# Kernel optimization log

Measured on AMD Instinct MI355X. Metric: run time of the kernel, lower is better.

## Reference

```python
import jax, jax.numpy as jnp
from jax import lax
import numpy as np

B, N, S, K = 8, 4096, 1024, 32
D_FEAT = 64
EPS = 1e-5


def fps_idx(pts, npoint):
    # pts: [N,3] -> farthest point sampling indices [npoint] (deterministic start at 0)
    n = pts.shape[0]
    def body(i, state):
        dist, far, idxs = state
        idxs = idxs.at[i].set(far)
        d = jnp.sum((pts - pts[far]) ** 2, axis=-1)
        dist = jnp.minimum(dist, d)
        return dist, jnp.argmax(dist).astype(jnp.int32), idxs
    init = (jnp.full((n,), 1e10, pts.dtype), jnp.int32(0), jnp.zeros((npoint,), jnp.int32))
    _, _, idxs = lax.fori_loop(0, npoint, body, init)
    return idxs


def bn(x, g, b, axes, c_axis):
    # batch-norm, training mode (batch statistics), matching torch default module state
    m = jnp.mean(x, axes, keepdims=True)
    v = jnp.var(x, axes, keepdims=True)
    shape = [1] * x.ndim
    shape[c_axis] = -1
    return g.reshape(shape) * (x - m) * lax.rsqrt(v + EPS) + b.reshape(shape)


def conv1x1(x, w, b):
    # x: [B,C,S,K], w: [O,C], b: [O]
    return jnp.einsum('oc,bcsk->bosk', w, x) + b[None, :, None, None]


def setup_inputs():
    key = jax.random.key(0)
    ks = jax.random.split(key, 20)
    p = lambda k, shape: jax.random.normal(k, shape, jnp.float32) * 0.05
    inp = {
        'xyz': jax.random.normal(ks[0], (B, 3, N), jnp.float32),
        'features': jax.random.normal(ks[1], (B, D_FEAT, N), jnp.float32),
        # main MLP: 67 -> 64 -> 64 -> 128
        'w0': p(ks[2], (64, 67)), 'b0': p(ks[3], (64,)), 'g0': jnp.ones(64), 'be0': jnp.zeros(64),
        'w1': p(ks[4], (64, 64)), 'b1': p(ks[5], (64,)), 'g1': jnp.ones(64), 'be1': jnp.zeros(64),
        'w2': p(ks[6], (128, 64)), 'b2': p(ks[7], (128,)), 'g2': jnp.ones(128), 'be2': jnp.zeros(128),
        # WeightNet: 3 -> 8 -> 8 -> 16
        'ww0': p(ks[8], (8, 3)), 'wb0': p(ks[9], (8,)), 'wg0': jnp.ones(8), 'wbe0': jnp.zeros(8),
        'ww1': p(ks[10], (8, 8)), 'wb1': p(ks[11], (8,)), 'wg1': jnp.ones(8), 'wbe1': jnp.zeros(8),
        'ww2': p(ks[12], (16, 8)), 'wb2': p(ks[13], (16,)), 'wg2': jnp.ones(16), 'wbe2': jnp.zeros(16),
        # final linear 16*128 -> 128 and BN1d
        'lw': p(ks[14], (128, 16 * 128)), 'lb': p(ks[15], (128,)),
        'lg': jnp.ones(128), 'lbe': jnp.zeros(128),
    }
    return inp


def reference(xyz, features, w0, b0, g0, be0, w1, b1, g1, be1, w2, b2, g2, be2,
              ww0, wb0, wg0, wbe0, ww1, wb1, wg1, wbe1, ww2, wb2, wg2, wbe2,
              lw, lb, lg, lbe):
    xyz_t = jnp.transpose(xyz, (0, 2, 1))          # [B,N,3]
    feat_t = jnp.transpose(features, (0, 2, 1))    # [B,N,D]

    # farthest point sampling (indices non-differentiable, as in CUDA FPS)
    fidx = jax.vmap(lambda pts: fps_idx(pts, S))(lax.stop_gradient(xyz_t))  # [B,S]
    fps_xyz = jnp.take_along_axis(xyz_t, fidx[..., None], axis=1)           # [B,S,3]

    # KNN: squared distances [B,S,N], take K smallest
    d2 = (jnp.sum(fps_xyz ** 2, -1, keepdims=True)
          + jnp.sum(xyz_t ** 2, -1)[:, None, :]
          - 2.0 * jnp.einsum('bsc,bnc->bsn', fps_xyz, xyz_t))
    _, idx = lax.top_k(-lax.stop_gradient(d2), K)                            # [B,S,K]

    gather = jax.vmap(lambda src, i: src[i])
    grouped_xyz = gather(xyz_t, idx) - fps_xyz[:, :, None, :]                # [B,S,K,3]
    grouped_feat = gather(feat_t, idx)                                       # [B,S,K,D]
    nf = jnp.concatenate([grouped_xyz, grouped_feat], axis=-1)               # [B,S,K,3+D]

    nf = jnp.transpose(nf, (0, 3, 1, 2))                                     # [B,C,S,K]
    for w, b, g, be in ((w0, b0, g0, be0), (w1, b1, g1, be1), (w2, b2, g2, be2)):
        nf = jax.nn.relu(bn(conv1x1(nf, w, b), g, be, (0, 2, 3), 1))

    gx = jnp.transpose(grouped_xyz, (0, 3, 1, 2))                            # [B,3,S,K]
    wts = gx
    for w, b, g, be in ((ww0, wb0, wg0, wbe0), (ww1, wb1, wg1, wbe1), (ww2, wb2, wg2, wbe2)):
        wts = jax.nn.relu(bn(conv1x1(wts, w, b), g, be, (0, 2, 3), 1))       # [B,16,S,K]

    agg = jnp.einsum('bdsk,bcsk->bsdc', nf, wts)                             # [B,S,128,16]
    agg = agg.reshape(agg.shape[0], agg.shape[1], -1)                        # [B,S,2048] (D outer, C inner)
    lin = agg @ lw.T + lb                                                    # [B,S,128]
    lin = jnp.transpose(lin, (0, 2, 1))                                      # [B,128,S]
    out_f = jax.nn.relu(bn(lin, lg, lbe, (0, 2), 1))

    new_xyz = jnp.transpose(fps_xyz, (0, 2, 1))                              # [B,3,S]
    return (new_xyz, out_f)
```

## Files before the change

kernel.cpp:

```cpp
#include <hip/hip_runtime.h>
#include <hip/hip_bf16.h>

#define BB 8
#define NN 4096
#define SS 1024
#define KK 32
#define PP (BB*SS*KK)

typedef unsigned long long u64;
typedef unsigned int u32;
typedef unsigned short u16;
typedef float f32x2 __attribute__((ext_vector_type(2)));

#define ST_Y0 0
#define ST_W0 64
#define ST_Y1 72
#define ST_W1 136
#define ST_Y2 144
#define ST_W2 272
#define ST_LIN 288

static __device__ __forceinline__ float bf2f(u32 u){ return __uint_as_float(u<<16); }
static __device__ __forceinline__ u16 f2bf(float f){ u32 u=__float_as_uint(f); return (u16)((u + 0x7FFFu + ((u>>16)&1u))>>16); }

static __device__ __forceinline__ f32x2 pk_add(f32x2 a, f32x2 b){
  f32x2 d; asm("v_pk_add_f32 %0, %1, %2" : "=v"(d) : "v"(a), "v"(b)); return d;
}
static __device__ __forceinline__ f32x2 pk_mul(f32x2 a, f32x2 b){
  f32x2 d; asm("v_pk_mul_f32 %0, %1, %2" : "=v"(d) : "v"(a), "v"(b)); return d;
}

static __device__ __forceinline__ uint4 pack8(const float* v){
  uint4 r;
  r.x=(u32)f2bf(v[0])|((u32)f2bf(v[1])<<16);
  r.y=(u32)f2bf(v[2])|((u32)f2bf(v[3])<<16);
  r.z=(u32)f2bf(v[4])|((u32)f2bf(v[5])<<16);
  r.w=(u32)f2bf(v[6])|((u32)f2bf(v[7])<<16);
  return r;
}

static __device__ __forceinline__ void unp8_aff(uint4 r, const float* A, const float* C, int cb, float* o){
  o[0]=fmaxf(fmaf(bf2f(r.x&0xffffu),A[cb+0],C[cb+0]),0.f);
  o[1]=fmaxf(fmaf(bf2f(r.x>>16)    ,A[cb+1],C[cb+1]),0.f);
  o[2]=fmaxf(fmaf(bf2f(r.y&0xffffu),A[cb+2],C[cb+2]),0.f);
  o[3]=fmaxf(fmaf(bf2f(r.y>>16)    ,A[cb+3],C[cb+3]),0.f);
  o[4]=fmaxf(fmaf(bf2f(r.z&0xffffu),A[cb+4],C[cb+4]),0.f);
  o[5]=fmaxf(fmaf(bf2f(r.z>>16)    ,A[cb+5],C[cb+5]),0.f);
  o[6]=fmaxf(fmaf(bf2f(r.w&0xffffu),A[cb+6],C[cb+6]),0.f);
  o[7]=fmaxf(fmaf(bf2f(r.w>>16)    ,A[cb+7],C[cb+7]),0.f);
}

template<int CTRL, int RMASK>
static __device__ __forceinline__ u32 dppmax(u32 m){
  u32 t=(u32)__builtin_amdgcn_update_dpp(0, (int)m, CTRL, RMASK, 0xf, false);
  return t>m ? t : m;
}
template<int CTRL, int RMASK>
static __device__ __forceinline__ float dppadd1(float v){
  float t=__uint_as_float((u32)__builtin_amdgcn_update_dpp(0,(int)__float_as_uint(v),CTRL,RMASK,0xf,false));
  return v+t;
}
static __device__ __forceinline__ float dppsum(float v){
  v=dppadd1<0x111,0xf>(v);
  v=dppadd1<0x112,0xf>(v);
  v=dppadd1<0x114,0xf>(v);
  v=dppadd1<0x118,0xf>(v);
  v=dppadd1<0x142,0xa>(v);
  v=dppadd1<0x143,0xc>(v);
  return v;
}
static __device__ __forceinline__ float rl63(float v){
  return __uint_as_float((u32)__builtin_amdgcn_readlane((int)__float_as_uint(v),63));
}

__global__ __launch_bounds__(256) void k_featT(const float* __restrict__ f, float* __restrict__ ft,
    const float* __restrict__ w0,const float* __restrict__ w1,const float* __restrict__ w2,
    const float* __restrict__ ww0,const float* __restrict__ ww1,const float* __restrict__ ww2,
    float* __restrict__ w0t,float* __restrict__ w1t,float* __restrict__ w2t,
    float* __restrict__ wt0,float* __restrict__ wt1,float* __restrict__ wt2,
    float* __restrict__ statsf){
  __shared__ float tile[64][65];
  if (blockIdx.x==512){
    int t=threadIdx.x;
    for (int i=t;i<1024;i+=256) statsf[i]=0.f;
    for (int i=t;i<64*67;i+=256){ int o=i/67,k=i%67; w0t[k*64+o]=w0[i]; }
    for (int i=t;i<64*64;i+=256){ int o=i>>6,k=i&63; w1t[k*64+o]=w1[i]; }
    for (int i=t;i<128*64;i+=256){ int o=i>>6,k=i&63; w2t[k*128+o]=w2[i]; }
    for (int i=t;i<8*3;i+=256){ int o=i/3,k=i%3; wt0[k*8+o]=ww0[i]; }
    for (int i=t;i<8*8;i+=256){ int o=i>>3,k=i&7; wt1[k*8+o]=ww1[i]; }
    for (int i=t;i<16*8;i+=256){ int o=i>>3,k=i&7; wt2[k*16+o]=ww2[i]; }
    return;
  }
  int b=blockIdx.x>>6; int n0=(blockIdx.x&63)*64;
  const float* fb=f+(size_t)b*64*NN;
  int c0=threadIdx.x>>6, nn=threadIdx.x&63;
  #pragma unroll
  for (int it=0;it<16;it++){ int c=c0+it*4; tile[c][nn]=fb[(size_t)c*NN+n0+nn]; }
  __syncthreads();
  int cc=threadIdx.x&63, n1=threadIdx.x>>6;
  float* fo=ft+((size_t)b*NN+n0)*64;
  #pragma unroll
  for (int it=0;it<16;it++){ int n=n1+it*4; fo[(size_t)n*64+cc]=tile[cc][n]; }
}

__global__ __launch_bounds__(512) void k_fps(const float* __restrict__ xyz,
                                             float* __restrict__ fpsq, float* __restrict__ outx){
  __shared__ float X[NN], Y[NN], Z[NN];
  __shared__ float QX[SS], QY[SS], QZ[SS];
  __shared__ u64 red[2][8];
  int b=blockIdx.x, t=threadIdx.x;
  const float* xb=xyz+(size_t)b*3*NN;
  for (int i=t;i<NN;i+=512){ X[i]=xb[i]; Y[i]=xb[NN+i]; Z[i]=xb[2*NN+i]; }
  __syncthreads();
  f32x2 px[4],py[4],pz[4],dd[4];
  #pragma unroll
  for (int k=0;k<4;k++){
    int i=t*8+2*k;
    px[k].x=X[i]; px[k].y=X[i+1];
    py[k].x=Y[i]; py[k].y=Y[i+1];
    pz[k].x=Z[i]; pz[k].y=Z[i+1];
    dd[k].x=1e10f; dd[k].y=1e10f;
  }
  int wv=t>>6, ln=t&63;
  int far=0;
  for (int s=0;s<SS;s++){
    float fx=X[far], fy=Y[far], fz=Z[far];
    if (t==0){ QX[s]=fx; QY[s]=fy; QZ[s]=fz; }
    f32x2 nfx, nfy, nfz;
    nfx.x=-fx; nfx.y=-fx; nfy.x=-fy; nfy.y=-fy; nfz.x=-fz; nfz.y=-fz;
    #pragma unroll
    for (int k=0;k<4;k++){
      f32x2 dx=pk_add(px[k],nfx);
      f32x2 xx=pk_mul(dx,dx);
      f32x2 dy=pk_add(py[k],nfy);
      f32x2 yy=pk_mul(dy,dy);
      f32x2 dz=pk_add(pz[k],nfz);
      f32x2 zz=pk_mul(dz,dz);
      f32x2 s1=pk_add(xx,yy);
      f32x2 d2=pk_add(s1,zz);
      dd[k].x=fminf(dd[k].x,d2.x);
      dd[k].y=fminf(dd[k].y,d2.y);
    }
    float m01=fmaxf(dd[0].x,dd[0].y), m23=fmaxf(dd[1].x,dd[1].y);
    float m45=fmaxf(dd[2].x,dd[2].y), m67=fmaxf(dd[3].x,dd[3].y);
    u32 m=__float_as_uint(fmaxf(fmaxf(m01,m23),fmaxf(m45,m67)));
    m=dppmax<0x111,0xf>(m);
    m=dppmax<0x112,0xf>(m);
    m=dppmax<0x114,0xf>(m);
    m=dppmax<0x118,0xf>(m);
    u32 r15=(u32)__builtin_amdgcn_readlane((int)m,15);
    u32 r31=(u32)__builtin_amdgcn_readlane((int)m,31);
    u32 r47=(u32)__builtin_amdgcn_readlane((int)m,47);
    u32 r63=(u32)__builtin_amdgcn_readlane((int)m,63);
    u32 ab = r15>r31 ? r15 : r31;
    u32 cd = r47>r63 ? r47 : r63;
    u32 wmax = ab>cd ? ab : cd;
    int lj=8;
    if (__float_as_uint(dd[3].y)==wmax) lj=7;
    if (__float_as_uint(dd[3].x)==wmax) lj=6;
    if (__float_as_uint(dd[2].y)==wmax) lj=5;
    if (__float_as_uint(dd[2].x)==wmax) lj=4;
    if (__float_as_uint(dd[1].y)==wmax) lj=3;
    if (__float_as_uint(dd[1].x)==wmax) lj=2;
    if (__float_as_uint(dd[0].y)==wmax) lj=1;
    if (__float_as_uint(dd[0].x)==wmax) lj=0;
    u64 ball=__ballot(lj<8);
    u32 wl=(u32)__builtin_ctzll(ball);
    int gi=t*8+lj;
    u32 widx=(u32)__builtin_amdgcn_readlane(gi,wl);
    int pb=s&1;
    if (ln==0) red[pb][wv]=((u64)wmax<<32)|(u32)(4095u-widx);
    __syncthreads();
    const double* rd=(const double*)&red[pb][0];
    double g=fmax(fmax(fmax(rd[0],rd[1]),fmax(rd[2],rd[3])),
                  fmax(fmax(rd[4],rd[5]),fmax(rd[6],rd[7])));
    far=4095-(int)(__double_as_longlong(g)&0xFFFull);
  }
  __syncthreads();
  for (int i=t;i<SS;i+=512){
    float qx=QX[i], qy=QY[i], qz=QZ[i];
    float* q=&fpsq[((size_t)b*SS+i)*3]; q[0]=qx; q[1]=qy; q[2]=qz;
    outx[b*3*SS+i]=qx; outx[b*3*SS+SS+i]=qy; outx[b*3*SS+2*SS+i]=qz;
  }
}

#define KSTR 68
__global__ __launch_bounds__(512) void k_knn(const float* __restrict__ xyz, const float* __restrict__ fpsq,
                                             int* __restrict__ kidx){
  extern __shared__ char smem[];
  float* xs=(float*)smem;
  float* ys=xs+64*KSTR;
  float* zs=ys+64*KSTR;
  float* pn=zs+64*KSTR;
  int blk=blockIdx.x; int b=blk>>7; int s0=(blk&127)*8;
  const float* xb=xyz+(size_t)b*3*NN;
  for (int i=threadIdx.x;i<NN;i+=512){
    float x=xb[i],y=xb[NN+i],z=xb[2*NN+i];
    int slot=(i>>6)*KSTR+(i&63);
    xs[slot]=x; ys[slot]=y; zs[slot]=z;
    pn[slot]=__fadd_rn(__fadd_rn(__fmul_rn(x,x),__fmul_rn(y,y)),__fmul_rn(z,z));
  }
  __syncthreads();
  int wv=threadIdx.x>>6, ln=threadIdx.x&63;
  int s=s0+wv;
  const float* q=&fpsq[((size_t)b*SS+s)*3];
  float qx=q[0],qy=q[1],qz=q[2];
  float qn=__fadd_rn(__fadd_rn(__fmul_rn(qx,qx),__fmul_rn(qy,qy)),__fmul_rn(qz,qz));
  f32x2 qxx,qyy,qzz,qnn,mtwo;
  qxx.x=qx;qxx.y=qx; qyy.x=qy;qyy.y=qy; qzz.x=qz;qzz.y=qz; qnn.x=qn;qnn.y=qn;
  mtwo.x=-2.f; mtwo.y=-2.f;
  const float4* Xp=(const float4*)(xs+ln*KSTR);
  const float4* Yp=(const float4*)(ys+ln*KSTR);
  const float4* Zp=(const float4*)(zs+ln*KSTR);
  const float4* Pp=(const float4*)(pn+ln*KSTR);
  int base=ln*64;
  u64 v[64];
  #pragma unroll
  for (int g=0;g<16;g++){
    float4 x4=Xp[g], y4=Yp[g], z4=Zp[g], p4=Pp[g];
    #pragma unroll
    for (int h=0;h<2;h++){
      f32x2 px2,py2,pz2,pn2;
      if (h==0){ px2.x=x4.x;px2.y=x4.y; py2.x=y4.x;py2.y=y4.y; pz2.x=z4.x;pz2.y=z4.y; pn2.x=p4.x;pn2.y=p4.y; }
      else     { px2.x=x4.z;px2.y=x4.w; py2.x=y4.z;py2.y=y4.w; pz2.x=z4.z;pz2.y=z4.w; pn2.x=p4.z;pn2.y=p4.w; }
      f32x2 m1=pk_mul(qxx,px2);
      f32x2 mm=pk_mul(qyy,py2);
      f32x2 a1=pk_add(m1,mm);
      f32x2 m3=pk_mul(qzz,pz2);
      f32x2 dt=pk_add(a1,m3);
      f32x2 qp=pk_add(qnn,pn2);
      f32x2 nd=pk_mul(dt,mtwo);
      f32x2 d2=pk_add(qp,nd);
      #pragma unroll
      for (int e=0;e<2;e++){
        u32 bu=__float_as_uint(e?d2.y:d2.x);
        bu = ((int)bu<0)? ~bu : (bu|0x80000000u);
        v[g*4+h*2+e]=((u64)bu<<32)|(u32)(base+g*4+h*2+e);
      }
    }
  }
  u64 cand[8];
  #pragma unroll
  for (int gg=0;gg<8;gg++){
    u64 c=v[gg*8];
    #pragma unroll
    for (int j=1;j<8;j++){ u64 x=v[gg*8+j]; c = x<c?x:c; }
    cand[gg]=c;
  }
  u64 best=cand[0];
  #pragma unroll
  for (int gg=1;gg<8;gg++){ u64 x=cand[gg]; best = x<best?x:best; }
  int my=0;
  #pragma unroll 1
  for (int r=0;r<KK;r++){
    u64 w=best;
    #pragma unroll
    for (int m=1;m<64;m<<=1){ u64 o=__shfl_xor(w,m,64); w = o<w?o:w; }
    if (ln==r) my=(int)(w&0xFFFull);
    if (best==w){
      #pragma unroll
      for (int gg=0;gg<8;gg++){
        if (cand[gg]==w){
          u64 c=~0ull;
          #pragma unroll
          for (int j=0;j<8;j++){ u64 x=v[gg*8+j]; x = x>w ? x : ~0ull; c = x<c?x:c; }
          cand[gg]=c;
        }
      }
      u64 nb=cand[0];
      #pragma unroll
      for (int gg=1;gg<8;gg++){ u64 x=cand[gg]; nb = x<nb?x:nb; }
      best=nb;
    }
  }
  if (ln<KK) kidx[(((size_t)b*SS+s)<<5)+ln]=my;
}

__global__ __launch_bounds__(256) void k_l0(const float* __restrict__ xyz, const float* __restrict__ ft,
    const float* __restrict__ fpsq, const int* __restrict__ kidx,
    const float* __restrict__ w0t, const float* __restrict__ wt0,
    u16* __restrict__ y0, float* __restrict__ wl0, float* __restrict__ statsf){
  __shared__ u16 ytile[256][64];
  __shared__ float pS[4][64], pQ[4][64];
  __shared__ float pWS[4][8], pWQ[4][8];
  int t=threadIdx.x; int wv=t>>6, ln=t&63;
  int p=blockIdx.x*256+t;
  int b=p>>15;
  int site=p>>5;
  int j=kidx[p];
  const float* xb=xyz+(size_t)b*3*NN;
  const float* q=fpsq+(size_t)site*3;
  float gx=xb[j]-q[0], gy=xb[NN+j]-q[1], gz=xb[2*NN+j]-q[2];
  float acc[64];
  #pragma unroll
  for (int c=0;c<64;c++) acc[c]=fmaf(gx,w0t[c],fmaf(gy,w0t[64+c],gz*w0t[128+c]));
  const float4* fr=(const float4*)(ft+((size_t)b*NN+j)*64);
  #pragma unroll 1
  for (int kb=0;kb<4;kb++){
    float4 r0=fr[kb*4+0], r1=fr[kb*4+1], r2=fr[kb*4+2], r3=fr[kb*4+3];
    float ch[16]={r0.x,r0.y,r0.z,r0.w,r1.x,r1.y,r1.z,r1.w,r2.x,r2.y,r2.z,r2.w,r3.x,r3.y,r3.z,r3.w};
    const float* wb=w0t+(3+kb*16)*64;
    #pragma unroll
    for (int kk=0;kk<16;kk++){
      #pragma unroll
      for (int c=0;c<64;c++) acc[c]=fmaf(ch[kk],wb[kk*64+c],acc[c]);
    }
  }
  u16* yr=y0+(size_t)p*64;
  #pragma unroll
  for (int c8=0;c8<8;c8++){
    uint4 pk=pack8(&acc[c8*8]);
    ((uint4*)yr)[c8]=pk;
    *((uint4*)&ytile[t][c8*8])=pk;
  }
  float wa[8];
  #pragma unroll
  for (int o=0;o<8;o++) wa[o]=fmaf(gx,wt0[o],fmaf(gy,wt0[8+o],gz*wt0[16+o]));
  float4* wr=(float4*)(wl0+(size_t)p*8);
  wr[0]=make_float4(wa[0],wa[1],wa[2],wa[3]);
  wr[1]=make_float4(wa[4],wa[5],wa[6],wa[7]);
  float wS[8],wQ[8];
  #pragma unroll
  for (int o=0;o<8;o++){
    wS[o]=rl63(dppsum(wa[o]));
    wQ[o]=rl63(dppsum(wa[o]*wa[o]));
  }
  if (ln==0){
    #pragma unroll
    for (int o=0;o<8;o++){ pWS[wv][o]=wS[o]; pWQ[wv][o]=wQ[o]; }
  }
  __syncthreads();
  {
    int c=t&63, rg=t>>6;
    float S=0.f,Q=0.f;
    #pragma unroll 16
    for (int r=0;r<64;r++){
      float v=bf2f((u32)ytile[rg*64+r][c]);
      S+=v; Q=fmaf(v,v,Q);
    }
    pS[rg][c]=S; pQ[rg][c]=Q;
  }
  __syncthreads();
  if (t<64){
    float S=pS[0][t]+pS[1][t]+pS[2][t]+pS[3][t];
    float Q=pQ[0][t]+pQ[1][t]+pQ[2][t]+pQ[3][t];
    atomicAdd(&statsf[2*(ST_Y0+t)],S); atomicAdd(&statsf[2*(ST_Y0+t)+1],Q);
  } else if (t<72){
    int c=t-64;
    float S=pWS[0][c]+pWS[1][c]+pWS[2][c]+pWS[3][c];
    float Q=pWQ[0][c]+pWQ[1][c]+pWQ[2][c]+pWQ[3][c];
    atomicAdd(&statsf[2*(ST_W0+c)],S); atomicAdd(&statsf[2*(ST_W0+c)+1],Q);
  }
}

__global__ __launch_bounds__(256) void k_l1(const u16* __restrict__ y0, const float* __restrict__ wl0,
    const float* __restrict__ w1t, const float* __restrict__ wt1,
    const float* __restrict__ statsf,
    const float* __restrict__ g0v, const float* __restrict__ be0v,
    const float* __restrict__ wg0v, const float* __restrict__ wbe0v,
    u16* __restrict__ y1, float* __restrict__ wl1, float* __restrict__ statso){
  __shared__ float A0[64],C0[64],AW[8],CW[8];
  __shared__ u16 ytile[256][64];
  __shared__ float pS[4][64], pQ[4][64];
  __shared__ float pWS[4][8], pWQ[4][8];
  int t=threadIdx.x; int wv=t>>6, ln=t&63;
  if (t<64){
    float sm=statsf[(ST_Y0+t)*2], sq=statsf[(ST_Y0+t)*2+1];
    float mean=sm*(1.f/PP), var=fmaxf(sq*(1.f/PP)-mean*mean,0.f);
    float a=g0v[t]*rsqrtf(var+1e-5f); A0[t]=a; C0[t]=be0v[t]-mean*a;
  } else if (t<72){
    int c=t-64;
    float sm=statsf[(ST_W0+c)*2], sq=statsf[(ST_W0+c)*2+1];
    float mean=sm*(1.f/PP), var=fmaxf(sq*(1.f/PP)-mean*mean,0.f);
    float a=wg0v[c]*rsqrtf(var+1e-5f); AW[c]=a; CW[c]=wbe0v[c]-mean*a;
  }
  __syncthreads();
  int p=blockIdx.x*256+t;
  const uint4* yr=(const uint4*)(y0+(size_t)p*64);
  float acc[64];
  #pragma unroll
  for (int c=0;c<64;c++) acc[c]=0.f;
  #pragma unroll 1
  for (int kb=0;kb<4;kb++){
    uint4 r0=yr[kb*2], r1=yr[kb*2+1];
    float ch[16];
    unp8_aff(r0,A0,C0,kb*16,ch);
    unp8_aff(r1,A0,C0,kb*16+8,ch+8);
    const float* wb=w1t+kb*16*64;
    #pragma unroll
    for (int kk=0;kk<16;kk++){
      #pragma unroll
      for (int c=0;c<64;c++) acc[c]=fmaf(ch[kk],wb[kk*64+c],acc[c]);
    }
  }
  u16* yo=y1+(size_t)p*64;
  #pragma unroll
  for (int c8=0;c8<8;c8++){
    uint4 pk=pack8(&acc[c8*8]);
    ((uint4*)yo)[c8]=pk;
    *((uint4*)&ytile[t][c8*8])=pk;
  }
  const float4* wvp=(const float4*)(wl0+(size_t)p*8);
  float4 v0=wvp[0], v1=wvp[1];
  float wi[8]={v0.x,v0.y,v0.z,v0.w,v1.x,v1.y,v1.z,v1.w};
  float wo[8];
  #pragma unroll
  for (int o=0;o<8;o++) wo[o]=0.f;
  #pragma unroll
  for (int k=0;k<8;k++){
    float xr=fmaxf(fmaf(wi[k],AW[k],CW[k]),0.f);
    #pragma unroll
    for (int o=0;o<8;o++) wo[o]=fmaf(xr,wt1[k*8+o],wo[o]);
  }
  float4* wr=(float4*)(wl1+(size_t)p*8);
  wr[0]=make_float4(wo[0],wo[1],wo[2],wo[3]);
  wr[1]=make_float4(wo[4],wo[5],wo[6],wo[7]);
  float wS[8],wQ[8];
  #pragma unroll
  for (int o=0;o<8;o++){
    wS[o]=rl63(dppsum(wo[o]));
    wQ[o]=rl63(dppsum(wo[o]*wo[o]));
  }
  if (ln==0){
    #pragma unroll
    for (int o=0;o<8;o++){ pWS[wv][o]=wS[o]; pWQ[wv][o]=wQ[o]; }
  }
  __syncthreads();
  {
    int c=t&63, rg=t>>6;
    float S=0.f,Q=0.f;
    #pragma unroll 16
    for (int r=0;r<64;r++){
      float v=bf2f((u32)ytile[rg*64+r][c]);
      S+=v; Q=fmaf(v,v,Q);
    }
    pS[rg][c]=S; pQ[rg][c]=Q;
  }
  __syncthreads();
  if (t<64){
    float S=pS[0][t]+pS[1][t]+pS[2][t]+pS[3][t];
    float Q=pQ[0][t]+pQ[1][t]+pQ[2][t]+pQ[3][t];
    atomicAdd(&statso[2*(ST_Y1+t)],S); atomicAdd(&statso[2*(ST_Y1+t)+1],Q);
  } else if (t<72){
    int c=t-64;
    float S=pWS[0][c]+pWS[1][c]+pWS[2][c]+pWS[3][c];
    float Q=pWQ[0][c]+pWQ[1][c]+pWQ[2][c]+pWQ[3][c];
    atomicAdd(&statso[2*(ST_W1+c)],S); atomicAdd(&statso[2*(ST_W1+c)+1],Q);
  }
}

__global__ __launch_bounds__(256) void k_l2(const u16* __restrict__ y1, const float* __restrict__ wl1,
    const float* __restrict__ w2t, const float* __restrict__ wt2,
    const float* __restrict__ statsf,
    const float* __restrict__ g1v, const float* __restrict__ be1v,
    const float* __restrict__ wg1v, const float* __restrict__ wbe1v,
    u16* __restrict__ y2, float* __restrict__ wl2, float* __restrict__ statso){
  __shared__ float A1[64],C1[64],AW[8],CW[8];
  __shared__ u16 ytile[256][64];
  __shared__ float pS[4][64], pQ[4][64];
  __shared__ float pWS[4][16], pWQ[4][16];
  int t=threadIdx.x; int wv=t>>6, ln=t&63;
  if (t<64){
    float sm=statsf[(ST_Y1+t)*2], sq=statsf[(ST_Y1+t)*2+1];
    float mean=sm*(1.f/PP), var=fmaxf(sq*(1.f/PP)-mean*mean,0.f);
    float a=g1v[t]*rsqrtf(var+1e-5f); A1[t]=a; C1[t]=be1v[t]-mean*a;
  } else if (t<72){
    int c=t-64;
    float sm=statsf[(ST_W1+c)*2], sq=statsf[(ST_W1+c)*2+1];
    float mean=sm*(1.f/PP), var=fmaxf(sq*(1.f/PP)-mean*mean,0.f);
    float a=wg1v[c]*rsqrtf(var+1e-5f); AW[c]=a; CW[c]=wbe1v[c]-mean*a;
  }
  __syncthreads();
  int p=blockIdx.x*256+t;
  const uint4* yr=(const uint4*)(y1+(size_t)p*64);
  #pragma unroll 1
  for (int h=0;h<2;h++){
    float acc[64];
    #pragma unroll
    for (int c=0;c<64;c++) acc[c]=0.f;
    #pragma unroll 1
    for (int kb=0;kb<4;kb++){
      uint4 r0=yr[kb*2], r1=yr[kb*2+1];
      float ch[16];
      unp8_aff(r0,A1,C1,kb*16,ch);
      unp8_aff(r1,A1,C1,kb*16+8,ch+8);
      const float* wb=w2t+(size_t)kb*16*128+h*64;
      #pragma unroll
      for (int kk=0;kk<16;kk++){
        #pragma unroll
        for (int c=0;c<64;c++) acc[c]=fmaf(ch[kk],wb[kk*128+c],acc[c]);
      }
    }
    u16* yo=y2+(size_t)p*128+h*64;
    #pragma unroll
    for (int c8=0;c8<8;c8++){
      uint4 pk=pack8(&acc[c8*8]);
      ((uint4*)yo)[c8]=pk;
      *((uint4*)&ytile[t][c8*8])=pk;
    }
    __syncthreads();
    {
      int c=t&63, rg=t>>6;
      float S=0.f,Q=0.f;
      #pragma unroll 16
      for (int r=0;r<64;r++){
        float v=bf2f((u32)ytile[rg*64+r][c]);
        S+=v; Q=fmaf(v,v,Q);
      }
      pS[rg][c]=S; pQ[rg][c]=Q;
    }
    __syncthreads();
    if (t<64){
      float S=pS[0][t]+pS[1][t]+pS[2][t]+pS[3][t];
      float Q=pQ[0][t]+pQ[1][t]+pQ[2][t]+pQ[3][t];
      atomicAdd(&statso[2*(ST_Y2+h*64+t)],S); atomicAdd(&statso[2*(ST_Y2+h*64+t)+1],Q);
    }
    __syncthreads();
  }
  const float4* wvp=(const float4*)(wl1+(size_t)p*8);
  float4 v0=wvp[0], v1=wvp[1];
  float wi[8]={v0.x,v0.y,v0.z,v0.w,v1.x,v1.y,v1.z,v1.w};
  float wo[16];
  #pragma unroll
  for (int o=0;o<16;o++) wo[o]=0.f;
  #pragma unroll
  for (int k=0;k<8;k++){
    float xr=fmaxf(fmaf(wi[k],AW[k],CW[k]),0.f);
    #pragma unroll
    for (int o=0;o<16;o++) wo[o]=fmaf(xr,wt2[k*16+o],wo[o]);
  }
  float4* wr=(float4*)(wl2+(size_t)p*16);
  wr[0]=make_float4(wo[0],wo[1],wo[2],wo[3]);
  wr[1]=make_float4(wo[4],wo[5],wo[6],wo[7]);
  wr[2]=make_float4(wo[8],wo[9],wo[10],wo[11]);
  wr[3]=make_float4(wo[12],wo[13],wo[14],wo[15]);
  float wS[16],wQ[16];
  #pragma unroll
  for (int o=0;o<16;o++){
    wS[o]=rl63(dppsum(wo[o]));
    wQ[o]=rl63(dppsum(wo[o]*wo[o]));
  }
  if (ln==0){
    #pragma unroll
    for (int o=0;o<16;o++){ pWS[wv][o]=wS[o]; pWQ[wv][o]=wQ[o]; }
  }
  __syncthreads();
  if (t<16){
    float S=pWS[0][t]+pWS[1][t]+pWS[2][t]+pWS[3][t];
    float Q=pWQ[0][t]+pWQ[1][t]+pWQ[2][t]+pWQ[3][t];
    atomicAdd(&statso[2*(ST_W2+t)],S); atomicAdd(&statso[2*(ST_W2+t)+1],Q);
  }
}

__global__ __launch_bounds__(256) void k_agg(const u16* __restrict__ y2, const float* __restrict__ wl2,
    const float* __restrict__ statsf,
    const float* __restrict__ g2v, const float* __restrict__ be2v,
    const float* __restrict__ wg2v, const float* __restrict__ wbe2v,
    u16* __restrict__ agg){
  __shared__ float A2[128],C2[128],AW[16],CW[16];
  __shared__ float nf[32*128];
  __shared__ float wt[32*16];
  int site=blockIdx.x; int t=threadIdx.x;
  if (t<128){
    float sm=statsf[(ST_Y2+t)*2], sq=statsf[(ST_Y2+t)*2+1];
    float mean=sm*(1.f/PP), var=fmaxf(sq*(1.f/PP)-mean*mean,0.f);
    float a=g2v[t]*rsqrtf(var+1e-5f); A2[t]=a; C2[t]=be2v[t]-mean*a;
  } else if (t<144){
    int c=t-128;
    float sm=statsf[(ST_W2+c)*2], sq=statsf[(ST_W2+c)*2+1];
    float mean=sm*(1.f/PP), var=fmaxf(sq*(1.f/PP)-mean*mean,0.f);
    float a=wg2v[c]*rsqrtf(var+1e-5f); AW[c]=a; CW[c]=wbe2v[c]-mean*a;
  }
  __syncthreads();
  const uint4* src=(const uint4*)(y2+(size_t)site*32*128);
  #pragma unroll
  for (int it=0;it<2;it++){
    int idx=t+it*256;
    uint4 r=src[idx];
    int base=(idx*8)&127; int kq=(idx*8)>>7;
    unp8_aff(r,A2,C2,base,&nf[kq*128+base]);
  }
  #pragma unroll
  for (int it=0;it<2;it++){
    int i=t+it*256;
    float x=wl2[(size_t)site*512+i]; int c=i&15;
    wt[i]=fmaxf(fmaf(x,AW[c],CW[c]),0.f);
  }
  __syncthreads();
  int d=t>>1, cb=(t&1)*8;
  float acc[8];
  #pragma unroll
  for (int e=0;e<8;e++) acc[e]=0.f;
  #pragma unroll 4
  for (int kq=0;kq<32;kq++){
    float nv=nf[kq*128+d];
    #pragma unroll
    for (int e=0;e<8;e++) acc[e]=fmaf(nv,wt[kq*16+cb+e],acc[e]);
  }
  ((uint4*)(agg+(size_t)site*2048))[t]=pack8(acc);
}

__global__ __launch_bounds__(256) void k_lin(const u16* __restrict__ agg, const float* __restrict__ lw,
                                             float* __restrict__ lin, float* __restrict__ outst){
  __shared__ float As[16][33];
  __shared__ float Bs[32][128];
  __shared__ float stS[8][132], stQ[8][132];
  int s0=blockIdx.x*16; int t=threadIdx.x;
  int tx=t&31, ty=t>>5;
  float a0[4]={0.f,0.f,0.f,0.f}, a1[4]={0.f,0.f,0.f,0.f};
  for (int kb=0;kb<2048;kb+=32){
    {
      int row=t>>4, kc=(t&15)*2;
      u32 raw=*(const u32*)(agg+((size_t)(s0+row))*2048+kb+kc);
      As[row][kc]=bf2f(raw&0xffffu); As[row][kc+1]=bf2f(raw>>16);
    }
    {
      int o=t>>1, ks=(t&1)*16;
      const float* lr=lw+(size_t)o*2048+kb+ks;
      #pragma unroll
      for (int i=0;i<16;i+=4){
        float4 r=*(const float4*)(lr+i);
        Bs[ks+i][o]=r.x; Bs[ks+i+1][o]=r.y; Bs[ks+i+2][o]=r.z; Bs[ks+i+3][o]=r.w;
      }
    }
    __syncthreads();
    #pragma unroll 8
    for (int kk=0;kk<32;kk++){
      float av0=As[ty*2][kk], av1=As[ty*2+1][kk];
      float4 bv=*(const float4*)(&Bs[kk][tx*4]);
      a0[0]=fmaf(av0,bv.x,a0[0]); a0[1]=fmaf(av0,bv.y,a0[1]);
      a0[2]=fmaf(av0,bv.z,a0[2]); a0[3]=fmaf(av0,bv.w,a0[3]);
      a1[0]=fmaf(av1,bv.x,a1[0]); a1[1]=fmaf(av1,bv.y,a1[1]);
      a1[2]=fmaf(av1,bv.z,a1[2]); a1[3]=fmaf(av1,bv.w,a1[3]);
    }
    __syncthreads();
  }
  *(float4*)(lin+((size_t)(s0+ty*2  ))*128+tx*4)=make_float4(a0[0],a0[1],a0[2],a0[3]);
  *(float4*)(lin+((size_t)(s0+ty*2+1))*128+tx*4)=make_float4(a1[0],a1[1],a1[2],a1[3]);
  #pragma unroll
  for (int j=0;j<4;j++){
    stS[ty][tx*4+j]=a0[j]+a1[j];
    stQ[ty][tx*4+j]=fmaf(a1[j],a1[j],a0[j]*a0[j]);
  }
  __syncthreads();
  if (t<128){
    float S=0.f,Q=0.f;
    #pragma unroll
    for (int k=0;k<8;k++){ S+=stS[k][t]; Q+=stQ[k][t]; }
    atomicAdd(&outst[2*t],S); atomicAdd(&outst[2*t+1],Q);
  }
}

__global__ __launch_bounds__(256) void k_out(const float* __restrict__ lin, const float* __restrict__ statsf,
    const float* __restrict__ lg, const float* __restrict__ lbe, float* __restrict__ outf){
  int t=blockIdx.x*256+threadIdx.x;
  int s4=(t&255)*4; int o=(t>>8)&127; int b=t>>15;
  float sm=statsf[(ST_LIN+o)*2], sq=statsf[(ST_LIN+o)*2+1];
  float mean=sm*(1.f/8192.f), var=fmaxf(sq*(1.f/8192.f)-mean*mean,0.f);
  float a=lg[o]*rsqrtf(var+1e-5f), cc=lbe[o]-mean*a;
  float v0=lin[((size_t)b*SS+s4+0)*128+o];
  float v1=lin[((size_t)b*SS+s4+1)*128+o];
  float v2=lin[((size_t)b*SS+s4+2)*128+o];
  float v3=lin[((size_t)b*SS+s4+3)*128+o];
  float4 r=make_float4(fmaxf(fmaf(v0,a,cc),0.f),fmaxf(fmaf(v1,a,cc),0.f),
                       fmaxf(fmaf(v2,a,cc),0.f),fmaxf(fmaf(v3,a,cc),0.f));
  *(float4*)(outf+((size_t)b*128+o)*SS+s4)=r;
}

extern "C" void kernel_launch(void* const* d_in, const int* in_sizes, int n_in,
                              void* d_out, int out_size, void* d_ws, size_t ws_size,
                              hipStream_t stream){
  (void)in_sizes;(void)n_in;(void)out_size;(void)ws_size;
  const float* xyz =(const float*)d_in[0];
  const float* feat=(const float*)d_in[1];
  const float* w0=(const float*)d_in[2];  const float* g0=(const float*)d_in[4];  const float* be0=(const float*)d_in[5];
  const float* w1=(const float*)d_in[6];  const float* g1=(const float*)d_in[8];  const float* be1=(const float*)d_in[9];
  const float* w2=(const float*)d_in[10]; const float* g2=(const float*)d_in[12]; const float* be2=(const float*)d_in[13];
  const float* ww0=(const float*)d_in[14]; const float* wg0=(const float*)d_in[16]; const float* wbe0=(const float*)d_in[17];
  const float* ww1=(const float*)d_in[18]; const float* wg1=(const float*)d_in[20]; const float* wbe1=(const float*)d_in[21];
  const float* ww2=(const float*)d_in[22]; const float* wg2=(const float*)d_in[24]; const float* wbe2=(const float*)d_in[25];
  const float* lw=(const float*)d_in[26]; const float* lg=(const float*)d_in[28]; const float* lbe=(const float*)d_in[29];
  float* out=(float*)d_out;
  char* ws=(char*)d_ws;

  size_t cur=0;
  auto alloc=[&](size_t bytes)->size_t{ cur=(cur+255)&~(size_t)255; size_t o=cur; cur+=bytes; return o; };
  size_t o_stats=alloc(4096);
  size_t o_w0t =alloc(67*64*4);
  size_t o_w1t =alloc(64*64*4);
  size_t o_w2t =alloc(64*128*4);
  size_t o_wt0 =alloc(3*8*4);
  size_t o_wt1 =alloc(8*8*4);
  size_t o_wt2 =alloc(8*16*4);
  size_t o_fpsq=alloc((size_t)BB*SS*3*4);
  size_t o_kidx=alloc((size_t)PP*4);
  size_t o_ft  =alloc((size_t)BB*NN*64*4);
  size_t o_y0  =alloc((size_t)PP*64*2);
  size_t o_y1  =alloc((size_t)PP*64*2);
  size_t o_y2  =alloc((size_t)PP*128*2);
  size_t o_wl0 =alloc((size_t)PP*8*4);
  size_t o_wl1 =alloc((size_t)PP*8*4);
  size_t o_wl2 =alloc((size_t)PP*16*4);
  size_t o_agg =alloc((size_t)8192*2048*2);
  size_t o_lin =alloc((size_t)8192*128*4);

  float* statsf=(float*)(ws+o_stats);
  float* w0t=(float*)(ws+o_w0t); float* w1t=(float*)(ws+o_w1t); float* w2t=(float*)(ws+o_w2t);
  float* wt0=(float*)(ws+o_wt0); float* wt1=(float*)(ws+o_wt1); float* wt2=(float*)(ws+o_wt2);
  float* fpsq=(float*)(ws+o_fpsq); int* kidx=(int*)(ws+o_kidx);
  float* ft=(float*)(ws+o_ft);
  u16* y0=(u16*)(ws+o_y0); u16* y1=(u16*)(ws+o_y1); u16* y2=(u16*)(ws+o_y2);
  float* wl0=(float*)(ws+o_wl0); float* wl1=(float*)(ws+o_wl1); float* wl2=(float*)(ws+o_wl2);
  u16* agg=(u16*)(ws+o_agg); float* lin=(float*)(ws+o_lin);

  size_t knn_smem = (size_t)4*64*KSTR*4;

  hipLaunchKernelGGL(k_featT,dim3(513),dim3(256),0,stream,feat,ft,
                     w0,w1,w2,ww0,ww1,ww2,w0t,w1t,w2t,wt0,wt1,wt2,statsf);
  hipLaunchKernelGGL(k_fps,dim3(BB),dim3(512),0,stream,xyz,fpsq,out);
  hipLaunchKernelGGL(k_knn,dim3(1024),dim3(512),knn_smem,stream,xyz,fpsq,kidx);
  hipLaunchKernelGGL(k_l0,dim3(PP/256),dim3(256),0,stream,xyz,ft,fpsq,kidx,w0t,wt0,y0,wl0,statsf);
  hipLaunchKernelGGL(k_l1,dim3(PP/256),dim3(256),0,stream,y0,wl0,w1t,wt1,statsf,g0,be0,wg0,wbe0,y1,wl1,statsf);
  hipLaunchKernelGGL(k_l2,dim3(PP/256),dim3(256),0,stream,y1,wl1,w2t,wt2,statsf,g1,be1,wg1,wbe1,y2,wl2,statsf);
  hipLaunchKernelGGL(k_agg,dim3(8192),dim3(256),0,stream,y2,wl2,statsf,g2,be2,wg2,wbe2,agg);
  hipLaunchKernelGGL(k_lin,dim3(512),dim3(256),0,stream,agg,lw,lin,statsf+2*ST_LIN);
  hipLaunchKernelGGL(k_out,dim3(1024),dim3(256),0,stream,lin,statsf,lg,lbe,out+BB*3*SS);
}
```

Before: 1.298 ms.

## Use bf16 MFMA for layer-1 and layer-2 pointwise convs with in-register stats

Replaces the per-thread scalar FMA matmuls in k_l1 and k_l2 with 16x16x32 bf16 MFMA tiles. Each block converts the raw weights to bf16 in LDS, and each wave normalizes 16-row activation slices into LDS before feeding the MFMAs. Batch-norm sums are accumulated from the MFMA outputs and reduced with shuffles, which removes the LDS ytile pass and the extra barriers. The trade-offs are per-block weight conversion, scattered 2-byte output stores, and a bf16 rounding of the normalized activations before the matmul.

```diff
diff --git a/kernel.cpp b/kernel.cpp
--- a/kernel.cpp
+++ b/kernel.cpp
@@ -11,6 +11,8 @@
 typedef unsigned int u32;
 typedef unsigned short u16;
 typedef float f32x2 __attribute__((ext_vector_type(2)));
+typedef float f32x4 __attribute__((ext_vector_type(4)));
+typedef short bf16x8 __attribute__((ext_vector_type(8)));
 
 #define ST_Y0 0
 #define ST_W0 64
@@ -28,6 +30,10 @@
 }
 static __device__ __forceinline__ f32x2 pk_mul(f32x2 a, f32x2 b){
   f32x2 d; asm("v_pk_mul_f32 %0, %1, %2" : "=v"(d) : "v"(a), "v"(b)); return d;
+}
+
+static __device__ __forceinline__ f32x4 mfma16(bf16x8 a, bf16x8 b, f32x4 c){
+  return __builtin_amdgcn_mfma_f32_16x16x32_bf16(a,b,c,0,0,0);
 }
 
 static __device__ __forceinline__ uint4 pack8(const float* v){
@@ -74,18 +80,15 @@
 }
 
 __global__ __launch_bounds__(256) void k_featT(const float* __restrict__ f, float* __restrict__ ft,
-    const float* __restrict__ w0,const float* __restrict__ w1,const float* __restrict__ w2,
-    const float* __restrict__ ww0,const float* __restrict__ ww1,const float* __restrict__ ww2,
-    float* __restrict__ w0t,float* __restrict__ w1t,float* __restrict__ w2t,
-    float* __restrict__ wt0,float* __restrict__ wt1,float* __restrict__ wt2,
+    const float* __restrict__ w0,const float* __restrict__ ww0,
+    float* __restrict__ w0t,float* __restrict__ wt0,float* __restrict__ wt1,float* __restrict__ wt2,
+    const float* __restrict__ ww1,const float* __restrict__ ww2,
     float* __restrict__ statsf){
   __shared__ float tile[64][65];
   if (blockIdx.x==512){
     int t=threadIdx.x;
     for (int i=t;i<1024;i+=256) statsf[i]=0.f;
     for (int i=t;i<64*67;i+=256){ int o=i/67,k=i%67; w0t[k*64+o]=w0[i]; }
-    for (int i=t;i<64*64;i+=256){ int o=i>>6,k=i&63; w1t[k*64+o]=w1[i]; }
-    for (int i=t;i<128*64;i+=256){ int o=i>>6,k=i&63; w2t[k*128+o]=w2[i]; }
     for (int i=t;i<8*3;i+=256){ int o=i/3,k=i%3; wt0[k*8+o]=ww0[i]; }
     for (int i=t;i<8*8;i+=256){ int o=i>>3,k=i&7; wt1[k*8+o]=ww1[i]; }
     for (int i=t;i<16*8;i+=256){ int o=i>>3,k=i&7; wt2[k*16+o]=ww2[i]; }
@@ -354,13 +357,14 @@
 }
 
 __global__ __launch_bounds__(256) void k_l1(const u16* __restrict__ y0, const float* __restrict__ wl0,
-    const float* __restrict__ w1t, const float* __restrict__ wt1,
+    const float* __restrict__ w1, const float* __restrict__ wt1,
     const float* __restrict__ statsf,
     const float* __restrict__ g0v, const float* __restrict__ be0v,
     const float* __restrict__ wg0v, const float* __restrict__ wbe0v,
     u16* __restrict__ y1, float* __restrict__ wl1, float* __restrict__ statso){
   __shared__ float A0[64],C0[64],AW[8],CW[8];
-  __shared__ u16 ytile[256][64];
+  __shared__ u16 Bw[64*72];
+  __shared__ u16 Atile[4][16*72];
   __shared__ float pS[4][64], pQ[4][64];
   __shared__ float pWS[4][8], pWQ[4][8];
   int t=threadIdx.x; int wv=t>>6, ln=t&63;
@@ -374,32 +378,58 @@
     float mean=sm*(1.f/PP), var=fmaxf(sq*(1.f/PP)-mean*mean,0.f);
     float a=wg0v[c]*rsqrtf(var+1e-5f); AW[c]=a; CW[c]=wbe0v[c]-mean*a;
   }
-  __syncthreads();
+  for (int i=t;i<4096;i+=256){ Bw[(i>>6)*72+(i&63)]=f2bf(w1[i]); }
+  __syncthreads();
+  bf16x8 bfr[4][2];
+  #pragma unroll
+  for (int n=0;n<4;n++){
+    const u16* bp=&Bw[(size_t)(n*16+(ln&15))*72 + (ln>>4)*8];
+    bfr[n][0]=*(const bf16x8*)bp;
+    bfr[n][1]=*(const bf16x8*)(bp+32);
+  }
+  float sS[4]={0,0,0,0}, sQ[4]={0,0,0,0};
+  int p0=blockIdx.x*256 + wv*64;
+  u16* At=Atile[wv];
+  #pragma unroll 1
+  for (int rs=0;rs<4;rs++){
+    int pr=p0+rs*16;
+    {
+      const u16* ysrc=y0+(size_t)pr*64 + ln*16;
+      uint4 raw0=*(const uint4*)ysrc;
+      uint4 raw1=*(const uint4*)(ysrc+8);
+      int row=ln>>2, cb=(ln&3)*16;
+      float tmp[8];
+      unp8_aff(raw0,A0,C0,cb,tmp);
+      *(uint4*)&At[row*72+cb]=pack8(tmp);
+      unp8_aff(raw1,A0,C0,cb+8,tmp);
+      *(uint4*)&At[row*72+cb+8]=pack8(tmp);
+    }
+    const u16* ap=&At[(ln&15)*72 + (ln>>4)*8];
+    bf16x8 a0=*(const bf16x8*)ap;
+    bf16x8 a1=*(const bf16x8*)(ap+32);
+    #pragma unroll
+    for (int n=0;n<4;n++){
+      f32x4 acc={0.f,0.f,0.f,0.f};
+      acc=mfma16(a0,bfr[n][0],acc);
+      acc=mfma16(a1,bfr[n][1],acc);
+      #pragma unroll
+      for (int i=0;i<4;i++){
+        int row=(ln>>4)*4+i;
+        y1[(size_t)(pr+row)*64 + n*16 + (ln&15)]=f2bf(acc[i]);
+        sS[n]+=acc[i]; sQ[n]=fmaf(acc[i],acc[i],sQ[n]);
+      }
+    }
+  }
+  #pragma unroll
+  for (int n=0;n<4;n++){
+    sS[n]+=__shfl_xor(sS[n],16,64); sS[n]+=__shfl_xor(sS[n],32,64);
+    sQ[n]+=__shfl_xor(sQ[n],16,64); sQ[n]+=__shfl_xor(sQ[n],32,64);
+  }
+  if (ln<16){
+    #pragma unroll
+    for (int n=0;n<4;n++){ pS[wv][n*16+ln]=sS[n]; pQ[wv][n*16+ln]=sQ[n]; }
+  }
   int p=blockIdx.x*256+t;
-  const uint4* yr=(const uint4*)(y0+(size_t)p*64);
-  float acc[64];
-  #pragma unroll
-  for (int c=0;c<64;c++) acc[c]=0.f;
-  #pragma unroll 1
-  for (int kb=0;kb<4;kb++){
-    uint4 r0=yr[kb*2], r1=yr[kb*2+1];
-    float ch[16];
-    unp8_aff(r0,A0,C0,kb*16,ch);
-    unp8_aff(r1,A0,C0,kb*16+8,ch+8);
-    const float* wb=w1t+kb*16*64;
-    #pragma unroll
-    for (int kk=0;kk<16;kk++){
-      #pragma unroll
-      for (int c=0;c<64;c++) acc[c]=fmaf(ch[kk],wb[kk*64+c],acc[c]);
-    }
-  }
-  u16* yo=y1+(size_t)p*64;
-  #pragma unroll
-  for (int c8=0;c8<8;c8++){
-    uint4 pk=pack8(&acc[c8*8]);
-    ((uint4*)yo)[c8]=pk;
-    *((uint4*)&ytile[t][c8*8])=pk;
-  }
   const float4* wvp=(const float4*)(wl0+(size_t)p*8);
   float4 v0=wvp[0], v1=wvp[1];
   float wi[8]={v0.x,v0.y,v0.z,v0.w,v1.x,v1.y,v1.z,v1.w};
@@ -424,17 +454,6 @@
   if (ln==0){
     #pragma unroll
     for (int o=0;o<8;o++){ pWS[wv][o]=wS[o]; pWQ[wv][o]=wQ[o]; }
-  }
-  __syncthreads();
-  {
-    int c=t&63, rg=t>>6;
-    float S=0.f,Q=0.f;
-    #pragma unroll 16
-    for (int r=0;r<64;r++){
-      float v=bf2f((u32)ytile[rg*64+r][c]);
-      S+=v; Q=fmaf(v,v,Q);
-    }
-    pS[rg][c]=S; pQ[rg][c]=Q;
   }
   __syncthreads();
   if (t<64){
@@ -450,14 +469,15 @@
 }
 
 __global__ __launch_bounds__(256) void k_l2(const u16* __restrict__ y1, const float* __restrict__ wl1,
-    const float* __restrict__ w2t, const float* __restrict__ wt2,
+    const float* __restrict__ w2, const float* __restrict__ wt2,
     const float* __restrict__ statsf,
     const float* __restrict__ g1v, const float* __restrict__ be1v,
     const float* __restrict__ wg1v, const float* __restrict__ wbe1v,
     u16* __restrict__ y2, float* __restrict__ wl2, float* __restrict__ statso){
   __shared__ float A1[64],C1[64],AW[8],CW[8];
-  __shared__ u16 ytile[256][64];
-  __shared__ float pS[4][64], pQ[4][64];
+  __shared__ u16 Bw[128*72];
+  __shared__ u16 Atile[4][16*72];
+  __shared__ float pS[4][128], pQ[4][128];
   __shared__ float pWS[4][16], pWQ[4][16];
   int t=threadIdx.x; int wv=t>>6, ln=t&63;
   if (t<64){
@@ -470,53 +490,54 @@
     float mean=sm*(1.f/PP), var=fmaxf(sq*(1.f/PP)-mean*mean,0.f);
     float a=wg1v[c]*rsqrtf(var+1e-5f); AW[c]=a; CW[c]=wbe1v[c]-mean*a;
   }
-  __syncthreads();
+  for (int i=t;i<8192;i+=256){ Bw[(i>>6)*72+(i&63)]=f2bf(w2[i]); }
+  __syncthreads();
+  float sS[8]={0,0,0,0,0,0,0,0}, sQ[8]={0,0,0,0,0,0,0,0};
+  int p0=blockIdx.x*256 + wv*64;
+  u16* At=Atile[wv];
+  #pragma unroll 1
+  for (int rs=0;rs<4;rs++){
+    int pr=p0+rs*16;
+    {
+      const u16* ysrc=y1+(size_t)pr*64 + ln*16;
+      uint4 raw0=*(const uint4*)ysrc;
+      uint4 raw1=*(const uint4*)(ysrc+8);
+      int row=ln>>2, cb=(ln&3)*16;
+      float tmp[8];
+      unp8_aff(raw0,A1,C1,cb,tmp);
+      *(uint4*)&At[row*72+cb]=pack8(tmp);
+      unp8_aff(raw1,A1,C1,cb+8,tmp);
+      *(uint4*)&At[row*72+cb+8]=pack8(tmp);
+    }
+    const u16* ap=&At[(ln&15)*72 + (ln>>4)*8];
+    bf16x8 a0=*(const bf16x8*)ap;
+    bf16x8 a1=*(const bf16x8*)(ap+32);
+    #pragma unroll
+    for (int n=0;n<8;n++){
+      const u16* bp=&Bw[(size_t)(n*16+(ln&15))*72 + (ln>>4)*8];
+      bf16x8 b0=*(const bf16x8*)bp;
+      bf16x8 b1=*(const bf16x8*)(bp+32);
+      f32x4 acc={0.f,0.f,0.f,0.f};
+      acc=mfma16(a0,b0,acc);
+      acc=mfma16(a1,b1,acc);
+      #pragma unroll
+      for (int i=0;i<4;i++){
+        int row=(ln>>4)*4+i;
+        y2[(size_t)(pr+row)*128 + n*16 + (ln&15)]=f2bf(acc[i]);
+        sS[n]+=acc[i]; sQ[n]=fmaf(acc[i],acc[i],sQ[n]);
+      }
+    }
+  }
+  #pragma unroll
+  for (int n=0;n<8;n++){
+    sS[n]+=__shfl_xor(sS[n],16,64); sS[n]+=__shfl_xor(sS[n],32,64);
+    sQ[n]+=__shfl_xor(sQ[n],16,64); sQ[n]+=__shfl_xor(sQ[n],32,64);
+  }
+  if (ln<16){
+    #pragma unroll
+    for (int n=0;n<8;n++){ pS[wv][n*16+ln]=sS[n]; pQ[wv][n*16+ln]=sQ[n]; }
+  }
   int p=blockIdx.x*256+t;
-  const uint4* yr=(const uint4*)(y1+(size_t)p*64);
-  #pragma unroll 1
-  for (int h=0;h<2;h++){
-    float acc[64];
-    #pragma unroll
-    for (int c=0;c<64;c++) acc[c]=0.f;
-    #pragma unroll 1
-    for (int kb=0;kb<4;kb++){
-      uint4 r0=yr[kb*2], r1=yr[kb*2+1];
-      float ch[16];
-      unp8_aff(r0,A1,C1,kb*16,ch);
-      unp8_aff(r1,A1,C1,kb*16+8,ch+8);
-      const float* wb=w2t+(size_t)kb*16*128+h*64;
-      #pragma unroll
-      for (int kk=0;kk<16;kk++){
-        #pragma unroll
-        for (int c=0;c<64;c++) acc[c]=fmaf(ch[kk],wb[kk*128+c],acc[c]);
-      }
-    }
-    u16* yo=y2+(size_t)p*128+h*64;
-    #pragma unroll
-    for (int c8=0;c8<8;c8++){
-      uint4 pk=pack8(&acc[c8*8]);
-      ((uint4*)yo)[c8]=pk;
-      *((uint4*)&ytile[t][c8*8])=pk;
-    }
-    __syncthreads();
-    {
-      int c=t&63, rg=t>>6;
-      float S=0.f,Q=0.f;
-      #pragma unroll 16
-      for (int r=0;r<64;r++){
-        float v=bf2f((u32)ytile[rg*64+r][c]);
-        S+=v; Q=fmaf(v,v,Q);
-      }
-      pS[rg][c]=S; pQ[rg][c]=Q;
-    }
-    __syncthreads();
-    if (t<64){
-      float S=pS[0][t]+pS[1][t]+pS[2][t]+pS[3][t];
-      float Q=pQ[0][t]+pQ[1][t]+pQ[2][t]+pQ[3][t];
-      atomicAdd(&statso[2*(ST_Y2+h*64+t)],S); atomicAdd(&statso[2*(ST_Y2+h*64+t)+1],Q);
-    }
-    __syncthreads();
-  }
   const float4* wvp=(const float4*)(wl1+(size_t)p*8);
   float4 v0=wvp[0], v1=wvp[1];
   float wi[8]={v0.x,v0.y,v0.z,v0.w,v1.x,v1.y,v1.z,v1.w};
@@ -545,10 +566,15 @@
     for (int o=0;o<16;o++){ pWS[wv][o]=wS[o]; pWQ[wv][o]=wQ[o]; }
   }
   __syncthreads();
-  if (t<16){
-    float S=pWS[0][t]+pWS[1][t]+pWS[2][t]+pWS[3][t];
-    float Q=pWQ[0][t]+pWQ[1][t]+pWQ[2][t]+pWQ[3][t];
-    atomicAdd(&statso[2*(ST_W2+t)],S); atomicAdd(&statso[2*(ST_W2+t)+1],Q);
+  if (t<128){
+    float S=pS[0][t]+pS[1][t]+pS[2][t]+pS[3][t];
+    float Q=pQ[0][t]+pQ[1][t]+pQ[2][t]+pQ[3][t];
+    atomicAdd(&statso[2*(ST_Y2+t)],S); atomicAdd(&statso[2*(ST_Y2+t)+1],Q);
+  } else if (t<144){
+    int c=t-128;
+    float S=pWS[0][c]+pWS[1][c]+pWS[2][c]+pWS[3][c];
+    float Q=pWQ[0][c]+pWQ[1][c]+pWQ[2][c]+pWQ[3][c];
+    atomicAdd(&statso[2*(ST_W2+c)],S); atomicAdd(&statso[2*(ST_W2+c)+1],Q);
   }
 }
 
@@ -687,8 +713,6 @@
   auto alloc=[&](size_t bytes)->size_t{ cur=(cur+255)&~(size_t)255; size_t o=cur; cur+=bytes; return o; };
   size_t o_stats=alloc(4096);
   size_t o_w0t =alloc(67*64*4);
-  size_t o_w1t =alloc(64*64*4);
-  size_t o_w2t =alloc(64*128*4);
   size_t o_wt0 =alloc(3*8*4);
   size_t o_wt1 =alloc(8*8*4);
   size_t o_wt2 =alloc(8*16*4);
@@ -705,7 +729,7 @@
   size_t o_lin =alloc((size_t)8192*128*4);
 
   float* statsf=(float*)(ws+o_stats);
-  float* w0t=(float*)(ws+o_w0t); float* w1t=(float*)(ws+o_w1t); float* w2t=(float*)(ws+o_w2t);
+  float* w0t=(float*)(ws+o_w0t);
   float* wt0=(float*)(ws+o_wt0); float* wt1=(float*)(ws+o_wt1); float* wt2=(float*)(ws+o_wt2);
   float* fpsq=(float*)(ws+o_fpsq); int* kidx=(int*)(ws+o_kidx);
   float* ft=(float*)(ws+o_ft);
@@ -716,12 +740,12 @@
   size_t knn_smem = (size_t)4*64*KSTR*4;
 
   hipLaunchKernelGGL(k_featT,dim3(513),dim3(256),0,stream,feat,ft,
-                     w0,w1,w2,ww0,ww1,ww2,w0t,w1t,w2t,wt0,wt1,wt2,statsf);
+                     w0,ww0,w0t,wt0,wt1,wt2,ww1,ww2,statsf);
   hipLaunchKernelGGL(k_fps,dim3(BB),dim3(512),0,stream,xyz,fpsq,out);
   hipLaunchKernelGGL(k_knn,dim3(1024),dim3(512),knn_smem,stream,xyz,fpsq,kidx);
   hipLaunchKernelGGL(k_l0,dim3(PP/256),dim3(256),0,stream,xyz,ft,fpsq,kidx,w0t,wt0,y0,wl0,statsf);
-  hipLaunchKernelGGL(k_l1,dim3(PP/256),dim3(256),0,stream,y0,wl0,w1t,wt1,statsf,g0,be0,wg0,wbe0,y1,wl1,statsf);
-  hipLaunchKernelGGL(k_l2,dim3(PP/256),dim3(256),0,stream,y1,wl1,w2t,wt2,statsf,g1,be1,wg1,wbe1,y2,wl2,statsf);
+  hipLaunchKernelGGL(k_l1,dim3(PP/256),dim3(256),0,stream,y0,wl0,w1,wt1,statsf,g0,be0,wg0,wbe0,y1,wl1,statsf);
+  hipLaunchKernelGGL(k_l2,dim3(PP/256),dim3(256),0,stream,y1,wl1,w2,wt2,statsf,g1,be1,wg1,wbe1,y2,wl2,statsf);
   hipLaunchKernelGGL(k_agg,dim3(8192),dim3(256),0,stream,y2,wl2,statsf,g2,be2,wg2,wbe2,agg);
   hipLaunchKernelGGL(k_lin,dim3(512),dim3(256),0,stream,agg,lw,lin,statsf+2*ST_LIN);
   hipLaunchKernelGGL(k_out,dim3(1024),dim3(256),0,stream,lin,statsf,lg,lbe,out+BB*3*SS);
```

New measurement: 1.177 ms. -9.3%, faster.
